# Kernel tuning notes

Hardware: AMD Instinct MI355X
Metric: run time of the kernel (lower is better)

## Reference

```python
import jax, jax.numpy as jnp
import numpy as np

A = 32           # num_atoms
R = A * (A - 1)  # num_rel (fully connected, no self loops)
B, T, D = 4, 64, 64
S, E = 4, 4      # num_states, edge_types
MH, MO, NH = 256, 256, 256

def _lrelu(x):
    return jax.nn.leaky_relu(x, 0.01)  # torch default slope

def setup_inputs() -> dict:
    key = jax.random.key(0)
    ks = jax.random.split(key, 16)
    # one-hot receiver/sender matrices for a fully connected graph
    off = np.ones((A, A)) - np.eye(A)
    rec_idx, send_idx = np.where(off)
    eye = np.eye(A, dtype=np.float32)
    rel_rec = jnp.asarray(eye[rec_idx])    # [R, A]
    rel_send = jnp.asarray(eye[send_idx])  # [R, A]
    w = 0.05
    return {
        "inputs": jax.random.normal(ks[0], (B, A, T, D), jnp.float32),
        "state": jax.random.uniform(ks[1], (B, A, T, S), jnp.float32),
        "rel_type": jax.random.uniform(ks[2], (B, R, S, E), jnp.float32),
        "rel_rec": rel_rec,
        "rel_send": rel_send,
        "msg_fc1_w": jax.random.normal(ks[3], (E, 2 * D, MH), jnp.float32) * w,
        "msg_fc1_b": jax.random.normal(ks[4], (E, MH), jnp.float32) * w,
        "msg_fc2_w": jax.random.normal(ks[5], (E, MH, MO), jnp.float32) * w,
        "msg_fc2_b": jax.random.normal(ks[6], (E, MO), jnp.float32) * w,
        "out_fc1_w": jax.random.normal(ks[7], (D + MO, NH), jnp.float32) * w,
        "out_fc1_b": jax.random.normal(ks[8], (NH,), jnp.float32) * w,
        "out_fc2_w": jax.random.normal(ks[9], (NH, NH), jnp.float32) * w,
        "out_fc2_b": jax.random.normal(ks[10], (NH,), jnp.float32) * w,
        "out_fc3_w": jax.random.normal(ks[11], (NH, D), jnp.float32) * w,
        "out_fc3_b": jax.random.normal(ks[12], (D,), jnp.float32) * w,
        "pred_steps": 1,
    }

def reference(inputs, state, rel_type, rel_rec, rel_send,
              msg_fc1_w, msg_fc1_b, msg_fc2_w, msg_fc2_b,
              out_fc1_w, out_fc1_b, out_fc2_w, out_fc2_b,
              out_fc3_w, out_fc3_b, pred_steps):
    # hidden_states=True, embedding=False, ball_pos=None, skip_first=True,
    # dropout p=0, pred_steps=1 -> one single_step_forward over all T.
    x = jnp.transpose(inputs, (0, 2, 1, 3))   # [B,T,A,D]
    st = jnp.transpose(state, (0, 2, 1, 3))   # [B,T,A,S]
    t = x.shape[1]

    # gather via one-hot matmuls
    recv = jnp.einsum('ra,btad->btrd', rel_rec, x)    # [B,T,R,D]
    send = jnp.einsum('ra,btad->btrd', rel_send, x)   # [B,T,R,D]
    ss = jnp.einsum('ra,btas->btrs', rel_send, st)    # [B,T,R,S]
    pre_msg = jnp.concatenate([send, recv], axis=-1)  # [B,T,R,2D]

    all_msgs = jnp.zeros(pre_msg.shape[:3] + (MO,), pre_msg.dtype)
    for i in range(1, E):  # skip_first_edge_type
        m = _lrelu(pre_msg @ msg_fc1_w[i] + msg_fc1_b[i])
        m = _lrelu(m @ msg_fc2_w[i] + msg_fc2_b[i])
        # gate: sum over states of rel_type[...,i] * sender states
        g = jnp.einsum('brs,btrs->btr', rel_type[..., i], ss)[..., None]
        all_msgs = all_msgs + m * g

    # scatter-accumulate messages back to receiver nodes
    agg = jnp.einsum('btrm,ra->btam', all_msgs, rel_rec)  # [B,T,A,MO]
    aug = jnp.concatenate([x, agg], axis=-1)              # skip_connection = inputs
    h = _lrelu(aug @ out_fc1_w + out_fc1_b)
    h = _lrelu(h @ out_fc2_w + out_fc2_b)
    pred = h @ out_fc3_w + out_fc3_b
    nxt = x + pred                                        # [B,T,A,D]

    out = nxt[:, : t - 1]                                 # pred_all
    return jnp.transpose(out, (0, 2, 1, 3))               # [B,A,T-1,D]
```

## Files before the change

kernel.cpp:

```cpp
#include <hip/hip_runtime.h>


typedef _Float16 f16x8 __attribute__((ext_vector_type(8)));
typedef float f32x4 __attribute__((ext_vector_type(4)));

#define MFMAH(a, b, c) __builtin_amdgcn_mfma_f32_16x16x32_f16((a), (b), (c), 0, 0, 0)

#define KBAR0() do {                                             \
  __builtin_amdgcn_sched_barrier(0);                             \
  asm volatile("s_waitcnt vmcnt(0) lgkmcnt(0)" ::: "memory");    \
  __builtin_amdgcn_s_barrier();                                  \
  __builtin_amdgcn_sched_barrier(0);                             \
} while (0)

__device__ __forceinline__ unsigned pkh(float lo, float hi) {
  auto h = __builtin_amdgcn_cvt_pkrtz(lo, hi);
  return __builtin_bit_cast(unsigned, h);
}
__device__ __forceinline__ unsigned short f2h(float f) {
  return __builtin_bit_cast(unsigned short, (_Float16)f);
}
__device__ __forceinline__ float lrelu(float x) { return x > 0.f ? x : 0.01f * x; }

__device__ __forceinline__ void gl16(const void* g, void* l) {
  __builtin_amdgcn_global_load_lds(
      (const __attribute__((address_space(1))) unsigned int*)(unsigned long long)g,
      (__attribute__((address_space(3))) unsigned int*)(unsigned int)(unsigned long long)l,
      16, 0, 0);
}

__global__ __launch_bounds__(256) void kw(
    const float* __restrict__ w1, const float* __restrict__ w2,
    const float* __restrict__ o1, const float* __restrict__ o2, const float* __restrict__ o3,
    unsigned short* __restrict__ W1T, unsigned short* __restrict__ W2F,
    unsigned short* __restrict__ O1T, unsigned short* __restrict__ O2T,
    unsigned short* __restrict__ O3T) {
  int i = blockIdx.x * 256 + threadIdx.x;
  if (i < 98304) {
    int k = i & 63, n = (i >> 6) & 255, eh = i >> 14;
    int e = (eh >> 1) + 1, half = eh & 1;
    W1T[i] = f2h(w1[(e * 128 + half * 64 + k) * 256 + n]);
    return;
  }
  i -= 98304;
  if (i < 196608) {
    int j = i & 7, l = (i >> 3) & 63, t = (i >> 9) & 15, s = (i >> 13) & 7, e = i >> 16;
    int n = t * 16 + (l & 15);
    int k = s * 32 + (l >> 4) * 8 + j;
    W2F[i] = f2h(w2[(e + 1) * 65536 + k * 256 + n]);
    return;
  }
  i -= 196608;
  if (i < 81920) {
    int k = i % 320, n = i / 320;
    O1T[i] = f2h(o1[k * 256 + n]);
    return;
  }
  i -= 81920;
  if (i < 65536) {
    int k = i & 255, n = i >> 8;
    O2T[i] = f2h(o2[k * 256 + n]);
    return;
  }
  i -= 65536;
  {
    int k = i & 255, n = i >> 8;
    O3T[i] = f2h(o3[k * 64 + n]);
  }
}

__global__ __launch_bounds__(256) void ka(
    const float* __restrict__ inputs, const float* __restrict__ state,
    const float* __restrict__ rel_type, const unsigned short* __restrict__ W1T,
    const float* __restrict__ b1g,
    unsigned short* __restrict__ P, float* __restrict__ G) {
  int t = blockIdx.x, b = blockIdx.y;
  int bt = b * 63 + t;
  int tid = threadIdx.x, lane = tid & 63, wid = tid >> 6;
  int waveM = wid & 1, waveN = wid >> 1;
  __shared__ __align__(16) _Float16 xa[32 * 72];
  __shared__ __align__(16) _Float16 Bt[256 * 72];
  __shared__ __align__(16) _Float16 Ps[32 * 256];
  __shared__ float ss[32][4];
  {
    int a = tid >> 3, d0 = (tid & 7) * 8;
    const float* src = inputs + (((b * 32 + a) * 64 + t) << 6) + d0;
    float4 v0 = *(const float4*)src;
    float4 v1 = *(const float4*)(src + 4);
    uint4 w;
    w.x = pkh(v0.x, v0.y); w.y = pkh(v0.z, v0.w);
    w.z = pkh(v1.x, v1.y); w.w = pkh(v1.z, v1.w);
    *(uint4*)&xa[a * 72 + d0] = w;
  }
  if (tid < 128) {
    int a = tid >> 2, s = tid & 3;
    ss[a][s] = state[((b * 32 + a) * 64 + t) * 4 + s];
  }
  __syncthreads();
  #pragma unroll
  for (int q = 0; q < 12; ++q) {
    int task = tid + q * 256;
    int e = task >> 10, rem = task & 1023, a = rem >> 5, k = rem & 31;
    float g = 0.f;
    if (k < 31) {
      int sA = k + (k >= a ? 1 : 0);
      int r = a * 31 + k;
      const float* rt = rel_type + (b * 992 + r) * 16 + (e + 1);
      g = rt[0] * ss[sA][0] + rt[4] * ss[sA][1] + rt[8] * ss[sA][2] + rt[12] * ss[sA][3];
    }
    G[(bt * 3 + e) * 1024 + a * 32 + k] = g;
  }
  for (int eh = 0; eh < 6; ++eh) {
    #pragma unroll
    for (int q = 0; q < 8; ++q) {
      int cid = tid + q * 256;
      int n = cid >> 3, c8 = (cid & 7) * 8;
      *(uint4*)&Bt[n * 72 + c8] = *(const uint4*)&W1T[(eh * 256 + n) * 64 + c8];
    }
    __syncthreads();
    f32x4 acc[8];
    #pragma unroll
    for (int f = 0; f < 8; ++f) acc[f] = f32x4{0.f, 0.f, 0.f, 0.f};
    #pragma unroll
    for (int ik = 0; ik < 2; ++ik) {
      int k0 = ik * 32;
      f16x8 av = *(const f16x8*)&xa[(waveM * 16 + (lane & 15)) * 72 + k0 + (lane >> 4) * 8];
      #pragma unroll
      for (int f = 0; f < 8; ++f) {
        f16x8 bv = *(const f16x8*)&Bt[(waveN * 128 + f * 16 + (lane & 15)) * 72 + k0 + (lane >> 4) * 8];
        acc[f] = MFMAH(av, bv, acc[f]);
      }
    }
    #pragma unroll
    for (int f = 0; f < 8; ++f) {
      int c = waveN * 128 + f * 16 + (lane & 15);
      float bias = (eh & 1) ? b1g[((eh >> 1) + 1) * 256 + c] : 0.f;
      #pragma unroll
      for (int i = 0; i < 4; ++i) {
        int rrow = waveM * 16 + (lane >> 4) * 4 + i;
        Ps[rrow * 256 + c] = (_Float16)(acc[f][i] + bias);
      }
    }
    __syncthreads();
    unsigned short* dst = P + (bt * 6 + eh) * 8192;
    #pragma unroll
    for (int q = 0; q < 4; ++q) {
      int o = (tid + q * 256) * 8;
      *(uint4*)&dst[o] = *(const uint4*)&Ps[o];
    }
    __syncthreads();
  }
}

__global__ __launch_bounds__(512, 4) void kb(
    const unsigned short* __restrict__ P, const float* __restrict__ G,
    const unsigned short* __restrict__ W2F, const float* __restrict__ b2g,
    unsigned short* __restrict__ AGG3) {
  int bx = blockIdx.x;
  int swz = (bx & 7) * 756 + (bx >> 3);
  int e = swz / 2016;
  int rem = swz - e * 2016;
  int bt = rem >> 3, q = rem & 7;
  int a0 = q * 4;
  int tid = threadIdx.x, lane = tid & 63, wid = tid >> 6;
  int waveM = wid & 1, waveN = wid >> 1;
  int lane15 = lane & 15, kqh = lane >> 4;

  __shared__ __align__(16) _Float16 h1F[2][4096];
  __shared__ __align__(16) _Float16 Bt[2][8192];
  __shared__ float gs[128];
  __shared__ float b2s[256];

  const unsigned short* psrc  = P + (bt * 6 + e * 2) * 8192;
  const unsigned short* prsrc = psrc + 8192;
  const unsigned short* w2f   = W2F + e * 65536;

  if (tid < 128) gs[tid] = G[((bt * 3 + e) << 10) + a0 * 32 + tid];
  if (tid >= 256 && tid < 512) b2s[tid - 256] = b2g[(e + 1) * 256 + (tid - 256)];

  int bm = tid >> 2, bch = tid & 3;
  int bal = bm >> 5, bk = bm & 31;
  int bs = (bk < 31) ? (bk + (bk >= a0 + bal ? 1 : 0)) : 0;
  const unsigned short* pvg = psrc + bs * 256 + bch * 8;
  const unsigned short* rvg = prsrc + (a0 + bal) * 256 + bch * 8;
  int h1off = (bm >> 4) * 512 + (bch * 16 + (bm & 15)) * 8;

  f32x4 acc[4][4];
  #pragma unroll
  for (int f = 0; f < 4; ++f)
    #pragma unroll
    for (int g2 = 0; g2 < 4; ++g2) acc[f][g2] = f32x4{0.f, 0.f, 0.f, 0.f};

  #pragma unroll
  for (int j = 0; j < 2; ++j) {
    int c = j * 512 + tid;
    gl16(w2f + c * 8, (char*)&Bt[0][0] + c * 16);
  }
  {
    f16x8 h = *(const f16x8*)(pvg) + *(const f16x8*)(rvg);
    *(f16x8*)&h1F[0][h1off] = __builtin_elementwise_max(h, h * (_Float16)0.01f);
  }
  KBAR0();

  #pragma unroll
  for (int step = 0; step < 8; ++step) {
    int buf = step & 1;
    if (step < 7) {
      f16x8 h = *(const f16x8*)(pvg + (step + 1) * 32) + *(const f16x8*)(rvg + (step + 1) * 32);
      *(f16x8*)&h1F[buf ^ 1][h1off] = __builtin_elementwise_max(h, h * (_Float16)0.01f);
      #pragma unroll
      for (int j = 0; j < 2; ++j) {
        int c = j * 512 + tid;
        gl16(w2f + (step + 1) * 8192 + c * 8, (char*)&Bt[buf ^ 1][0] + c * 16);
      }
    }
    f16x8 af[4];
    #pragma unroll
    for (int f = 0; f < 4; ++f)
      af[f] = *(const f16x8*)&h1F[buf][(waveM * 4 + f) * 512 + lane * 8];
    __builtin_amdgcn_s_setprio(1);
    #pragma unroll
    for (int g2 = 0; g2 < 4; ++g2) {
      f16x8 bv = *(const f16x8*)&Bt[buf][(waveN * 4 + g2) * 512 + lane * 8];
      #pragma unroll
      for (int f = 0; f < 4; ++f)
        acc[f][g2] = MFMAH(af[f], bv, acc[f][g2]);
    }
    __builtin_amdgcn_s_setprio(0);
    if (step < 7) KBAR0();
  }

  _Float16* aggh = (_Float16*)AGG3;
  #pragma unroll
  for (int half = 0; half < 2; ++half) {
    int al = waveM * 2 + half;
    #pragma unroll
    for (int g2 = 0; g2 < 4; ++g2) {
      int c = waveN * 64 + g2 * 16 + lane15;
      float bb = b2s[c];
      float p = 0.f;
      #pragma unroll
      for (int fh = 0; fh < 2; ++fh) {
        int f = half * 2 + fh;
        int k4 = fh * 16 + kqh * 4;
        #pragma unroll
        for (int i = 0; i < 4; ++i)
          p += gs[al * 32 + k4 + i] * lrelu(acc[f][g2][i] + bb);
      }
      p += __shfl_xor(p, 16, 64);
      p += __shfl_xor(p, 32, 64);
      if (lane < 16)
        aggh[(size_t)e * 2064384 + (((bt * 32 + a0 + al) << 8) + c)] = (_Float16)p;
    }
  }
}

__global__ __launch_bounds__(256) void kc(
    const float* __restrict__ inputs, const unsigned short* __restrict__ AGG3,
    const unsigned short* __restrict__ O1T, const unsigned short* __restrict__ O2T,
    const unsigned short* __restrict__ O3T,
    const float* __restrict__ ob1, const float* __restrict__ ob2, const float* __restrict__ ob3,
    float* __restrict__ out) {
  int t = blockIdx.x, b = blockIdx.y;
  int bt = b * 63 + t;
  int tid = threadIdx.x, lane = tid & 63, wid = tid >> 6;
  int waveM = wid & 1, waveN = wid >> 1;
  __shared__ __align__(16) _Float16 aug[32 * 328];
  __shared__ __align__(16) _Float16 h1[32 * 264];
  __shared__ __align__(16) _Float16 h2[32 * 264];
  __shared__ __align__(16) _Float16 Bt[256 * 40];
  __shared__ __align__(16) float xs[32 * 64];
  __shared__ float lb1[256], lb2[256], lb3[64];
  {
    int a = tid >> 3, d0 = (tid & 7) * 8;
    const float* src = inputs + (((b * 32 + a) * 64 + t) << 6) + d0;
    float4 v0 = *(const float4*)src;
    float4 v1 = *(const float4*)(src + 4);
    *(float4*)&xs[a * 64 + d0] = v0;
    *(float4*)&xs[a * 64 + d0 + 4] = v1;
    uint4 w;
    w.x = pkh(v0.x, v0.y); w.y = pkh(v0.z, v0.w);
    w.z = pkh(v1.x, v1.y); w.w = pkh(v1.z, v1.w);
    *(uint4*)&aug[a * 328 + d0] = w;
  }
  #pragma unroll
  for (int qq = 0; qq < 4; ++qq) {
    int cid = tid + qq * 256;
    int a = cid >> 5, c8 = (cid & 31) * 8;
    size_t o = ((size_t)(bt * 32 + a) << 8) + c8;
    f16x8 v0 = *(const f16x8*)&AGG3[o];
    f16x8 v1 = *(const f16x8*)&AGG3[2064384 + o];
    f16x8 v2 = *(const f16x8*)&AGG3[4128768 + o];
    f16x8 s = v0 + v1 + v2;
    *(uint4*)&aug[a * 328 + 64 + c8] = __builtin_bit_cast(uint4, s);
  }
  lb1[tid] = ob1[tid];
  lb2[tid] = ob2[tid];
  if (tid < 64) lb3[tid] = ob3[tid];
  __syncthreads();
  f32x4 acc[8];
  #pragma unroll
  for (int f = 0; f < 8; ++f) acc[f] = f32x4{0.f, 0.f, 0.f, 0.f};
  for (int kk = 0; kk < 10; ++kk) {
    #pragma unroll
    for (int q = 0; q < 4; ++q) {
      int cid = tid + q * 256;
      int n = cid >> 2, c8 = (cid & 3) * 8;
      *(uint4*)&Bt[n * 40 + c8] = *(const uint4*)&O1T[n * 320 + kk * 32 + c8];
    }
    __syncthreads();
    f16x8 av = *(const f16x8*)&aug[(waveM * 16 + (lane & 15)) * 328 + kk * 32 + (lane >> 4) * 8];
    #pragma unroll
    for (int f = 0; f < 8; ++f) {
      f16x8 bv = *(const f16x8*)&Bt[(waveN * 128 + f * 16 + (lane & 15)) * 40 + (lane >> 4) * 8];
      acc[f] = MFMAH(av, bv, acc[f]);
    }
    __syncthreads();
  }
  #pragma unroll
  for (int f = 0; f < 8; ++f) {
    int c = waveN * 128 + f * 16 + (lane & 15);
    #pragma unroll
    for (int i = 0; i < 4; ++i) {
      int r = waveM * 16 + (lane >> 4) * 4 + i;
      h1[r * 264 + c] = (_Float16)lrelu(acc[f][i] + lb1[c]);
    }
  }
  __syncthreads();
  #pragma unroll
  for (int f = 0; f < 8; ++f) acc[f] = f32x4{0.f, 0.f, 0.f, 0.f};
  for (int kk = 0; kk < 8; ++kk) {
    #pragma unroll
    for (int q = 0; q < 4; ++q) {
      int cid = tid + q * 256;
      int n = cid >> 2, c8 = (cid & 3) * 8;
      *(uint4*)&Bt[n * 40 + c8] = *(const uint4*)&O2T[n * 256 + kk * 32 + c8];
    }
    __syncthreads();
    f16x8 av = *(const f16x8*)&h1[(waveM * 16 + (lane & 15)) * 264 + kk * 32 + (lane >> 4) * 8];
    #pragma unroll
    for (int f = 0; f < 8; ++f) {
      f16x8 bv = *(const f16x8*)&Bt[(waveN * 128 + f * 16 + (lane & 15)) * 40 + (lane >> 4) * 8];
      acc[f] = MFMAH(av, bv, acc[f]);
    }
    __syncthreads();
  }
  #pragma unroll
  for (int f = 0; f < 8; ++f) {
    int c = waveN * 128 + f * 16 + (lane & 15);
    #pragma unroll
    for (int i = 0; i < 4; ++i) {
      int r = waveM * 16 + (lane >> 4) * 4 + i;
      h2[r * 264 + c] = (_Float16)lrelu(acc[f][i] + lb2[c]);
    }
  }
  __syncthreads();
  f32x4 a3[2];
  a3[0] = f32x4{0.f, 0.f, 0.f, 0.f};
  a3[1] = f32x4{0.f, 0.f, 0.f, 0.f};
  for (int kk = 0; kk < 8; ++kk) {
    {
      int n = tid >> 2, c8 = (tid & 3) * 8;
      *(uint4*)&Bt[n * 40 + c8] = *(const uint4*)&O3T[n * 256 + kk * 32 + c8];
    }
    __syncthreads();
    f16x8 av = *(const f16x8*)&h2[(waveM * 16 + (lane & 15)) * 264 + kk * 32 + (lane >> 4) * 8];
    #pragma unroll
    for (int f = 0; f < 2; ++f) {
      f16x8 bv = *(const f16x8*)&Bt[(waveN * 32 + f * 16 + (lane & 15)) * 40 + (lane >> 4) * 8];
      a3[f] = MFMAH(av, bv, a3[f]);
    }
    __syncthreads();
  }
  #pragma unroll
  for (int f = 0; f < 2; ++f) {
    int d = waveN * 32 + f * 16 + (lane & 15);
    #pragma unroll
    for (int i = 0; i < 4; ++i) {
      int a = waveM * 16 + (lane >> 4) * 4 + i;
      out[((b * 32 + a) * 63 + t) * 64 + d] = a3[f][i] + lb3[d] + xs[a * 64 + d];
    }
  }
}

extern "C" void kernel_launch(void* const* d_in, const int* in_sizes, int n_in,
                              void* d_out, int out_size, void* d_ws, size_t ws_size,
                              hipStream_t stream) {
  const float* inputs   = (const float*)d_in[0];
  const float* state    = (const float*)d_in[1];
  const float* rel_type = (const float*)d_in[2];
  const float* w1  = (const float*)d_in[5];
  const float* b1  = (const float*)d_in[6];
  const float* w2  = (const float*)d_in[7];
  const float* b2  = (const float*)d_in[8];
  const float* o1w = (const float*)d_in[9];
  const float* o1b = (const float*)d_in[10];
  const float* o2w = (const float*)d_in[11];
  const float* o2b = (const float*)d_in[12];
  const float* o3w = (const float*)d_in[13];
  const float* o3b = (const float*)d_in[14];
  char* ws = (char*)d_ws;
  unsigned short* W1T = (unsigned short*)(ws + 0);
  unsigned short* W2F = (unsigned short*)(ws + 196608);
  unsigned short* O1T = (unsigned short*)(ws + 589824);
  unsigned short* O2T = (unsigned short*)(ws + 753664);
  unsigned short* O3T = (unsigned short*)(ws + 884736);
  unsigned short* Pp  = (unsigned short*)(ws + 917504);
  float* G    = (float*)(ws + 25690112);
  unsigned short* AGG3 = (unsigned short*)(ws + 28786688);
  float* out = (float*)d_out;

  kw<<<1792, 256, 0, stream>>>(w1, w2, o1w, o2w, o3w, W1T, W2F, O1T, O2T, O3T);
  ka<<<dim3(63, 4), 256, 0, stream>>>(inputs, state, rel_type, W1T, b1, Pp, G);
  kb<<<6048, 512, 0, stream>>>(Pp, G, W2F, b2, AGG3);
  kc<<<dim3(63, 4), 256, 0, stream>>>(inputs, AGG3, O1T, O2T, O3T, o1b, o2b, o3b, out);
}
```

Before: 169.0 us.

## Keep full fc2 weight resident in LDS and loop all atom groups per block

Each kb block now loads the entire 256x256 f16 fc2 weight slice for its edge type into LDS once, then loops over all 8 receiver-atom groups for its (b,t). This replaces 6048 blocks that each streamed the weight in double-buffered chunks with 756 blocks, removing repeated weight traffic and per-step global-to-LDS loads, and the barriers now wait only on LDS counters. The cost is 128KB+ of LDS per block, which lowers occupancy (launch bounds drop to 2), and fewer blocks with longer serial loops, leaving less parallelism to hide latency.

```diff
diff --git a/kernel.cpp b/kernel.cpp
--- a/kernel.cpp
+++ b/kernel.cpp
@@ -9,6 +9,13 @@
 #define KBAR0() do {                                             \
   __builtin_amdgcn_sched_barrier(0);                             \
   asm volatile("s_waitcnt vmcnt(0) lgkmcnt(0)" ::: "memory");    \
+  __builtin_amdgcn_s_barrier();                                  \
+  __builtin_amdgcn_sched_barrier(0);                             \
+} while (0)
+
+#define KBARL() do {                                             \
+  __builtin_amdgcn_sched_barrier(0);                             \
+  asm volatile("s_waitcnt lgkmcnt(0)" ::: "memory");             \
   __builtin_amdgcn_s_barrier();                                  \
   __builtin_amdgcn_sched_barrier(0);                             \
 } while (0)
@@ -152,106 +159,113 @@
   }
 }
 
-__global__ __launch_bounds__(512, 4) void kb(
+__global__ __launch_bounds__(512, 2) void kb(
     const unsigned short* __restrict__ P, const float* __restrict__ G,
     const unsigned short* __restrict__ W2F, const float* __restrict__ b2g,
     unsigned short* __restrict__ AGG3) {
   int bx = blockIdx.x;
-  int swz = (bx & 7) * 756 + (bx >> 3);
-  int e = swz / 2016;
-  int rem = swz - e * 2016;
-  int bt = rem >> 3, q = rem & 7;
-  int a0 = q * 4;
+  int e = bx / 252;
+  int bt = bx - e * 252;
   int tid = threadIdx.x, lane = tid & 63, wid = tid >> 6;
   int waveM = wid & 1, waveN = wid >> 1;
   int lane15 = lane & 15, kqh = lane >> 4;
 
+  __shared__ __align__(16) _Float16 Bt[65536];
   __shared__ __align__(16) _Float16 h1F[2][4096];
-  __shared__ __align__(16) _Float16 Bt[2][8192];
-  __shared__ float gs[128];
+  __shared__ float gs[1024];
   __shared__ float b2s[256];
 
   const unsigned short* psrc  = P + (bt * 6 + e * 2) * 8192;
   const unsigned short* prsrc = psrc + 8192;
   const unsigned short* w2f   = W2F + e * 65536;
 
-  if (tid < 128) gs[tid] = G[((bt * 3 + e) << 10) + a0 * 32 + tid];
-  if (tid >= 256 && tid < 512) b2s[tid - 256] = b2g[(e + 1) * 256 + (tid - 256)];
-
-  int bm = tid >> 2, bch = tid & 3;
-  int bal = bm >> 5, bk = bm & 31;
-  int bs = (bk < 31) ? (bk + (bk >= a0 + bal ? 1 : 0)) : 0;
-  const unsigned short* pvg = psrc + bs * 256 + bch * 8;
-  const unsigned short* rvg = prsrc + (a0 + bal) * 256 + bch * 8;
-  int h1off = (bm >> 4) * 512 + (bch * 16 + (bm & 15)) * 8;
+  #pragma unroll
+  for (int j = 0; j < 16; ++j) {
+    int c = j * 512 + tid;
+    gl16(w2f + c * 8, (char*)&Bt[0] + c * 16);
+  }
+  int gofs = (bt * 3 + e) << 10;
+  gs[tid] = G[gofs + tid];
+  gs[512 + tid] = G[gofs + 512 + tid];
+  if (tid < 256) b2s[tid] = b2g[(e + 1) * 256 + tid];
+
+  int rrow = wid * 16 + lane15;
+  int al0 = rrow >> 5, bk = rrow & 31;
+  {
+    int bs = (bk < 31) ? bk + (bk >= al0 ? 1 : 0) : 0;
+    int ko = kqh * 8;
+    f16x8 h = *(const f16x8*)(psrc + bs * 256 + ko) + *(const f16x8*)(prsrc + al0 * 256 + ko);
+    *(f16x8*)&h1F[0][wid * 512 + lane * 8] = __builtin_elementwise_max(h, h * (_Float16)0.01f);
+  }
+  KBAR0();
 
   f32x4 acc[4][4];
-  #pragma unroll
-  for (int f = 0; f < 4; ++f)
-    #pragma unroll
-    for (int g2 = 0; g2 < 4; ++g2) acc[f][g2] = f32x4{0.f, 0.f, 0.f, 0.f};
-
-  #pragma unroll
-  for (int j = 0; j < 2; ++j) {
-    int c = j * 512 + tid;
-    gl16(w2f + c * 8, (char*)&Bt[0][0] + c * 16);
-  }
-  {
-    f16x8 h = *(const f16x8*)(pvg) + *(const f16x8*)(rvg);
-    *(f16x8*)&h1F[0][h1off] = __builtin_elementwise_max(h, h * (_Float16)0.01f);
-  }
-  KBAR0();
-
-  #pragma unroll
-  for (int step = 0; step < 8; ++step) {
-    int buf = step & 1;
-    if (step < 7) {
-      f16x8 h = *(const f16x8*)(pvg + (step + 1) * 32) + *(const f16x8*)(rvg + (step + 1) * 32);
-      *(f16x8*)&h1F[buf ^ 1][h1off] = __builtin_elementwise_max(h, h * (_Float16)0.01f);
-      #pragma unroll
-      for (int j = 0; j < 2; ++j) {
-        int c = j * 512 + tid;
-        gl16(w2f + (step + 1) * 8192 + c * 8, (char*)&Bt[buf ^ 1][0] + c * 16);
-      }
-    }
-    f16x8 af[4];
+  _Float16* aggh = (_Float16*)AGG3;
+
+  for (int it = 0; it < 8; ++it) {
+    int a0 = it * 4;
     #pragma unroll
     for (int f = 0; f < 4; ++f)
-      af[f] = *(const f16x8*)&h1F[buf][(waveM * 4 + f) * 512 + lane * 8];
-    __builtin_amdgcn_s_setprio(1);
-    #pragma unroll
-    for (int g2 = 0; g2 < 4; ++g2) {
-      f16x8 bv = *(const f16x8*)&Bt[buf][(waveN * 4 + g2) * 512 + lane * 8];
+      #pragma unroll
+      for (int g2 = 0; g2 < 4; ++g2) acc[f][g2] = f32x4{0.f, 0.f, 0.f, 0.f};
+
+    #pragma unroll
+    for (int s = 0; s < 8; ++s) {
+      int buf = s & 1;
+      bool hasNext = (s < 7) || (it < 7);
+      f16x8 pv, rv;
+      if (hasNext) {
+        int a0n = (s < 7) ? a0 : a0 + 4;
+        int sn = (s < 7) ? s + 1 : 0;
+        int bs = (bk < 31) ? bk + (bk >= a0n + al0 ? 1 : 0) : 0;
+        int ko = sn * 32 + kqh * 8;
+        pv = *(const f16x8*)(psrc + bs * 256 + ko);
+        rv = *(const f16x8*)(prsrc + (a0n + al0) * 256 + ko);
+      }
+      f16x8 af[4];
       #pragma unroll
       for (int f = 0; f < 4; ++f)
-        acc[f][g2] = MFMAH(af[f], bv, acc[f][g2]);
-    }
-    __builtin_amdgcn_s_setprio(0);
-    if (step < 7) KBAR0();
-  }
-
-  _Float16* aggh = (_Float16*)AGG3;
-  #pragma unroll
-  for (int half = 0; half < 2; ++half) {
-    int al = waveM * 2 + half;
-    #pragma unroll
-    for (int g2 = 0; g2 < 4; ++g2) {
-      int c = waveN * 64 + g2 * 16 + lane15;
-      float bb = b2s[c];
-      float p = 0.f;
-      #pragma unroll
-      for (int fh = 0; fh < 2; ++fh) {
-        int f = half * 2 + fh;
-        int k4 = fh * 16 + kqh * 4;
+        af[f] = *(const f16x8*)&h1F[buf][(waveM * 4 + f) * 512 + lane * 8];
+      __builtin_amdgcn_s_setprio(1);
+      #pragma unroll
+      for (int g2 = 0; g2 < 4; ++g2) {
+        f16x8 bv = *(const f16x8*)&Bt[(s * 16 + waveN * 4 + g2) * 512 + lane * 8];
         #pragma unroll
-        for (int i = 0; i < 4; ++i)
-          p += gs[al * 32 + k4 + i] * lrelu(acc[f][g2][i] + bb);
-      }
-      p += __shfl_xor(p, 16, 64);
-      p += __shfl_xor(p, 32, 64);
-      if (lane < 16)
-        aggh[(size_t)e * 2064384 + (((bt * 32 + a0 + al) << 8) + c)] = (_Float16)p;
-    }
+        for (int f = 0; f < 4; ++f)
+          acc[f][g2] = MFMAH(af[f], bv, acc[f][g2]);
+      }
+      __builtin_amdgcn_s_setprio(0);
+      if (hasNext) {
+        f16x8 h = pv + rv;
+        *(f16x8*)&h1F[buf ^ 1][wid * 512 + lane * 8] =
+            __builtin_elementwise_max(h, h * (_Float16)0.01f);
+      }
+      if (s < 7) KBARL();
+    }
+
+    #pragma unroll
+    for (int half = 0; half < 2; ++half) {
+      int al = waveM * 2 + half;
+      #pragma unroll
+      for (int g2 = 0; g2 < 4; ++g2) {
+        int c = waveN * 64 + g2 * 16 + lane15;
+        float bb = b2s[c];
+        float p = 0.f;
+        #pragma unroll
+        for (int fh = 0; fh < 2; ++fh) {
+          int f = half * 2 + fh;
+          int k4 = fh * 16 + kqh * 4;
+          #pragma unroll
+          for (int i = 0; i < 4; ++i)
+            p += gs[(a0 + al) * 32 + k4 + i] * lrelu(acc[f][g2][i] + bb);
+        }
+        p += __shfl_xor(p, 16, 64);
+        p += __shfl_xor(p, 32, 64);
+        if (lane < 16)
+          aggh[(size_t)e * 2064384 + (((bt * 32 + a0 + al) << 8) + c)] = (_Float16)p;
+      }
+    }
+    if (it < 7) KBARL();
   }
 }
 
@@ -412,6 +426,6 @@
 
   kw<<<1792, 256, 0, stream>>>(w1, w2, o1w, o2w, o3w, W1T, W2F, O1T, O2T, O3T);
   ka<<<dim3(63, 4), 256, 0, stream>>>(inputs, state, rel_type, W1T, b1, Pp, G);
-  kb<<<6048, 512, 0, stream>>>(Pp, G, W2F, b2, AGG3);
+  kb<<<756, 512, 0, stream>>>(Pp, G, W2F, b2, AGG3);
   kc<<<dim3(63, 4), 256, 0, stream>>>(inputs, AGG3, O1T, O2T, O3T, o1b, o2b, o3b, out);
 }
```

Result: slower. 181.5 us (+7.4%).

## Triple-buffer W2 tiles and defer h1 writes to overlap global loads with MFMA

Applied to the files above, without the earlier changes.

Raises the W2 LDS staging from double to triple buffering, so the weight tile is prefetched two steps ahead. The step barrier now waits on a partial vmcnt instead of draining every outstanding global load. The h1 activation loads are issued before the MFMAs and only combined and written to LDS after them, which hides their latency behind compute. The per-thread mapping for the h1 gather is also reorganized per wave. The extra Bt buffer raises LDS use and may lower occupancy, and correctness depends on the vmcnt counting being exact.

```diff
diff --git a/kernel.cpp b/kernel.cpp
--- a/kernel.cpp
+++ b/kernel.cpp
@@ -9,6 +9,13 @@
 #define KBAR0() do {                                             \
   __builtin_amdgcn_sched_barrier(0);                             \
   asm volatile("s_waitcnt vmcnt(0) lgkmcnt(0)" ::: "memory");    \
+  __builtin_amdgcn_s_barrier();                                  \
+  __builtin_amdgcn_sched_barrier(0);                             \
+} while (0)
+
+#define KBARL() do {                                             \
+  __builtin_amdgcn_sched_barrier(0);                             \
+  asm volatile("s_waitcnt lgkmcnt(0)" ::: "memory");             \
   __builtin_amdgcn_s_barrier();                                  \
   __builtin_amdgcn_sched_barrier(0);                             \
 } while (0)
@@ -167,7 +174,7 @@
   int lane15 = lane & 15, kqh = lane >> 4;
 
   __shared__ __align__(16) _Float16 h1F[2][4096];
-  __shared__ __align__(16) _Float16 Bt[2][8192];
+  __shared__ __align__(16) _Float16 Bt[3][8192];
   __shared__ float gs[128];
   __shared__ float b2s[256];
 
@@ -175,15 +182,29 @@
   const unsigned short* prsrc = psrc + 8192;
   const unsigned short* w2f   = W2F + e * 65536;
 
-  if (tid < 128) gs[tid] = G[((bt * 3 + e) << 10) + a0 * 32 + tid];
-  if (tid >= 256 && tid < 512) b2s[tid - 256] = b2g[(e + 1) * 256 + (tid - 256)];
-
-  int bm = tid >> 2, bch = tid & 3;
-  int bal = bm >> 5, bk = bm & 31;
-  int bs = (bk < 31) ? (bk + (bk >= a0 + bal ? 1 : 0)) : 0;
-  const unsigned short* pvg = psrc + bs * 256 + bch * 8;
-  const unsigned short* rvg = prsrc + (a0 + bal) * 256 + bch * 8;
-  int h1off = (bm >> 4) * 512 + (bch * 16 + (bm & 15)) * 8;
+  int rrow = wid * 16 + lane15;
+  int al0 = rrow >> 5, bk = rrow & 31;
+  int bs = (bk < 31) ? bk + (bk >= a0 + al0 ? 1 : 0) : 0;
+  const unsigned short* pvg = psrc + bs * 256 + kqh * 8;
+  const unsigned short* rvg = prsrc + (a0 + al0) * 256 + kqh * 8;
+  int h1off = wid * 512 + lane * 8;
+
+  {
+    f16x8 pv = *(const f16x8*)(pvg);
+    f16x8 rv = *(const f16x8*)(rvg);
+    __builtin_amdgcn_sched_barrier(0);
+    #pragma unroll
+    for (int j = 0; j < 2; ++j) {
+      int c = j * 512 + tid;
+      gl16(w2f + c * 8, (char*)&Bt[0][0] + c * 16);
+      gl16(w2f + 8192 + c * 8, (char*)&Bt[1][0] + c * 16);
+    }
+    if (tid < 128) gs[tid] = G[((bt * 3 + e) << 10) + a0 * 32 + tid];
+    if (tid >= 256) b2s[tid - 256] = b2g[(e + 1) * 256 + (tid - 256)];
+    f16x8 h = pv + rv;
+    *(f16x8*)&h1F[0][h1off] = __builtin_elementwise_max(h, h * (_Float16)0.01f);
+  }
+  KBAR0();
 
   f32x4 acc[4][4];
   #pragma unroll
@@ -192,26 +213,19 @@
     for (int g2 = 0; g2 < 4; ++g2) acc[f][g2] = f32x4{0.f, 0.f, 0.f, 0.f};
 
   #pragma unroll
-  for (int j = 0; j < 2; ++j) {
-    int c = j * 512 + tid;
-    gl16(w2f + c * 8, (char*)&Bt[0][0] + c * 16);
-  }
-  {
-    f16x8 h = *(const f16x8*)(pvg) + *(const f16x8*)(rvg);
-    *(f16x8*)&h1F[0][h1off] = __builtin_elementwise_max(h, h * (_Float16)0.01f);
-  }
-  KBAR0();
-
-  #pragma unroll
-  for (int step = 0; step < 8; ++step) {
-    int buf = step & 1;
-    if (step < 7) {
-      f16x8 h = *(const f16x8*)(pvg + (step + 1) * 32) + *(const f16x8*)(rvg + (step + 1) * 32);
-      *(f16x8*)&h1F[buf ^ 1][h1off] = __builtin_elementwise_max(h, h * (_Float16)0.01f);
+  for (int s = 0; s < 8; ++s) {
+    const int buf = s & 1;
+    f16x8 pv, rv;
+    if (s < 7) {
+      pv = *(const f16x8*)(pvg + (s + 1) * 32);
+      rv = *(const f16x8*)(rvg + (s + 1) * 32);
+    }
+    __builtin_amdgcn_sched_barrier(0);
+    if (s < 6) {
       #pragma unroll
       for (int j = 0; j < 2; ++j) {
         int c = j * 512 + tid;
-        gl16(w2f + (step + 1) * 8192 + c * 8, (char*)&Bt[buf ^ 1][0] + c * 16);
+        gl16(w2f + (s + 2) * 8192 + c * 8, (char*)&Bt[(s + 2) % 3][0] + c * 16);
       }
     }
     f16x8 af[4];
@@ -221,13 +235,19 @@
     __builtin_amdgcn_s_setprio(1);
     #pragma unroll
     for (int g2 = 0; g2 < 4; ++g2) {
-      f16x8 bv = *(const f16x8*)&Bt[buf][(waveN * 4 + g2) * 512 + lane * 8];
+      f16x8 bv = *(const f16x8*)&Bt[s % 3][(waveN * 4 + g2) * 512 + lane * 8];
       #pragma unroll
       for (int f = 0; f < 4; ++f)
         acc[f][g2] = MFMAH(af[f], bv, acc[f][g2]);
     }
     __builtin_amdgcn_s_setprio(0);
-    if (step < 7) KBAR0();
+    if (s < 7) {
+      f16x8 h = pv + rv;
+      *(f16x8*)&h1F[buf ^ 1][h1off] = __builtin_elementwise_max(h, h * (_Float16)0.01f);
+      if (s < 6)
+        asm volatile("s_waitcnt vmcnt(2)" ::: "memory");
+      KBARL();
+    }
   }
 
   _Float16* aggh = (_Float16*)AGG3;
```

Result: faster. 165.0 us (-2.4%).

## Build A fragments in registers from global and triple-buffer weight tiles

Applied to the files above, without the earlier changes.

Each wave now loads its sender and receiver rows from global memory straight into MFMA A-fragment registers and applies add plus leaky-ReLU there, so the h1F shared staging buffer and its LDS write/read round trip go away. The weight tiles move to a three-slot LDS ring that is prefetched two steps ahead. The per-step barrier now waits only on lgkmcnt, relying on the in-order vmcnt wait for the A-fragment loads to also cover the earlier weight prefetch. In exchange, global memory is read redundantly across waves, the code leans on that implicit ordering, and LDS use per block grows.

```diff
diff --git a/kernel.cpp b/kernel.cpp
--- a/kernel.cpp
+++ b/kernel.cpp
@@ -166,8 +166,7 @@
   int waveM = wid & 1, waveN = wid >> 1;
   int lane15 = lane & 15, kqh = lane >> 4;
 
-  __shared__ __align__(16) _Float16 h1F[2][4096];
-  __shared__ __align__(16) _Float16 Bt[2][8192];
+  __shared__ __align__(16) _Float16 Bt[3][8192];
   __shared__ float gs[128];
   __shared__ float b2s[256];
 
@@ -175,59 +174,73 @@
   const unsigned short* prsrc = psrc + 8192;
   const unsigned short* w2f   = W2F + e * 65536;
 
-  if (tid < 128) gs[tid] = G[((bt * 3 + e) << 10) + a0 * 32 + tid];
-  if (tid >= 256 && tid < 512) b2s[tid - 256] = b2g[(e + 1) * 256 + (tid - 256)];
-
-  int bm = tid >> 2, bch = tid & 3;
-  int bal = bm >> 5, bk = bm & 31;
-  int bs = (bk < 31) ? (bk + (bk >= a0 + bal ? 1 : 0)) : 0;
-  const unsigned short* pvg = psrc + bs * 256 + bch * 8;
-  const unsigned short* rvg = prsrc + (a0 + bal) * 256 + bch * 8;
-  int h1off = (bm >> 4) * 512 + (bch * 16 + (bm & 15)) * 8;
-
-  f32x4 acc[4][4];
-  #pragma unroll
-  for (int f = 0; f < 4; ++f)
-    #pragma unroll
-    for (int g2 = 0; g2 < 4; ++g2) acc[f][g2] = f32x4{0.f, 0.f, 0.f, 0.f};
+  int pOffB[4];
+  #pragma unroll
+  for (int f = 0; f < 4; ++f) {
+    int r = (waveM * 4 + f) * 16 + lane15;
+    int al = r >> 5, bk = r & 31;
+    int bs = (bk < 31) ? (bk + (bk >= a0 + al ? 1 : 0)) : 0;
+    pOffB[f] = (bs * 256 + kqh * 8) * 2;
+  }
+  const char* pbase = (const char*)psrc;
+  const unsigned short* rbase = prsrc + (a0 + waveM * 2) * 256 + kqh * 8;
 
   #pragma unroll
   for (int j = 0; j < 2; ++j) {
     int c = j * 512 + tid;
     gl16(w2f + c * 8, (char*)&Bt[0][0] + c * 16);
-  }
-  {
-    f16x8 h = *(const f16x8*)(pvg) + *(const f16x8*)(rvg);
-    *(f16x8*)&h1F[0][h1off] = __builtin_elementwise_max(h, h * (_Float16)0.01f);
-  }
+    gl16(w2f + 8192 + c * 8, (char*)&Bt[1][0] + c * 16);
+  }
+  if (tid < 128) gs[tid] = G[((bt * 3 + e) << 10) + a0 * 32 + tid];
+  if (tid >= 256 && tid < 512) b2s[tid - 256] = b2g[(e + 1) * 256 + (tid - 256)];
   KBAR0();
 
-  #pragma unroll
-  for (int step = 0; step < 8; ++step) {
-    int buf = step & 1;
-    if (step < 7) {
-      f16x8 h = *(const f16x8*)(pvg + (step + 1) * 32) + *(const f16x8*)(rvg + (step + 1) * 32);
-      *(f16x8*)&h1F[buf ^ 1][h1off] = __builtin_elementwise_max(h, h * (_Float16)0.01f);
+  f32x4 acc[4][4];
+  #pragma unroll
+  for (int f = 0; f < 4; ++f)
+    #pragma unroll
+    for (int g2 = 0; g2 < 4; ++g2) acc[f][g2] = f32x4{0.f, 0.f, 0.f, 0.f};
+
+  #pragma unroll
+  for (int s = 0; s < 8; ++s) {
+    f16x8 bv[4];
+    #pragma unroll
+    for (int g2 = 0; g2 < 4; ++g2)
+      bv[g2] = *(const f16x8*)&Bt[s % 3][(waveN * 4 + g2) * 512 + lane * 8];
+    __builtin_amdgcn_sched_barrier(0);
+    f16x8 af[4];
+    #pragma unroll
+    for (int fh = 0; fh < 2; ++fh) {
+      f16x8 rv = *(const f16x8*)(rbase + fh * 256 + s * 32);
+      f16x8 pa = *(const f16x8*)(pbase + pOffB[2 * fh]     + s * 64);
+      f16x8 pb = *(const f16x8*)(pbase + pOffB[2 * fh + 1] + s * 64);
+      f16x8 ha = pa + rv;
+      f16x8 hb = pb + rv;
+      af[2 * fh]     = __builtin_elementwise_max(ha, ha * (_Float16)0.01f);
+      af[2 * fh + 1] = __builtin_elementwise_max(hb, hb * (_Float16)0.01f);
+    }
+    __builtin_amdgcn_sched_barrier(0);
+    if (s < 6) {
       #pragma unroll
       for (int j = 0; j < 2; ++j) {
         int c = j * 512 + tid;
-        gl16(w2f + (step + 1) * 8192 + c * 8, (char*)&Bt[buf ^ 1][0] + c * 16);
+        gl16(w2f + (s + 2) * 8192 + c * 8, (char*)&Bt[(s + 2) % 3][0] + c * 16);
       }
     }
-    f16x8 af[4];
-    #pragma unroll
-    for (int f = 0; f < 4; ++f)
-      af[f] = *(const f16x8*)&h1F[buf][(waveM * 4 + f) * 512 + lane * 8];
+    __builtin_amdgcn_sched_barrier(0);
     __builtin_amdgcn_s_setprio(1);
     #pragma unroll
-    for (int g2 = 0; g2 < 4; ++g2) {
-      f16x8 bv = *(const f16x8*)&Bt[buf][(waveN * 4 + g2) * 512 + lane * 8];
+    for (int g2 = 0; g2 < 4; ++g2)
       #pragma unroll
       for (int f = 0; f < 4; ++f)
-        acc[f][g2] = MFMAH(af[f], bv, acc[f][g2]);
-    }
+        acc[f][g2] = MFMAH(af[f], bv[g2], acc[f][g2]);
     __builtin_amdgcn_s_setprio(0);
-    if (step < 7) KBAR0();
+    if (s < 7) {
+      __builtin_amdgcn_sched_barrier(0);
+      asm volatile("s_waitcnt lgkmcnt(0)" ::: "memory");
+      __builtin_amdgcn_s_barrier();
+      __builtin_amdgcn_sched_barrier(0);
+    }
   }
 
   _Float16* aggh = (_Float16*)AGG3;
```

After: 278.1 us. +64.6%, slower.
